# Kernel optimization log

Hardware: AMD Instinct MI355X
Metric: run time of the kernel (lower is better)

Reference implementation:

```python
import jax, jax.numpy as jnp
import numpy as np


def _lstm(x, Wk, Wr, b, reverse, return_seq):
    # Keras LSTM with activation='relu', recurrent_activation='sigmoid'.
    # Wk: (F, 4H), Wr: (H, 4H), b: (4H). Gate order: i, f, c, o.
    if reverse:
        x = jnp.flip(x, 1)
    H = Wr.shape[0]
    xg = jnp.einsum('btf,fg->btg', x, Wk) + b  # (B, T, 4H)
    B = x.shape[0]

    def step(carry, g_t):
        h, c = carry
        g = g_t + h @ Wr
        i = jax.nn.sigmoid(g[:, :H])
        f = jax.nn.sigmoid(g[:, H:2 * H])
        cc = jax.nn.relu(g[:, 2 * H:3 * H])
        o = jax.nn.sigmoid(g[:, 3 * H:])
        c = f * c + i * cc
        h = o * jax.nn.relu(c)
        return (h, c), h

    init = (jnp.zeros((B, H), x.dtype), jnp.zeros((B, H), x.dtype))
    (h, _), hs = jax.lax.scan(step, init, jnp.swapaxes(xg, 0, 1))
    if return_seq:
        hs = jnp.swapaxes(hs, 0, 1)  # (B, T, H)
        if reverse:
            hs = jnp.flip(hs, 1)
        return hs
    return h


def setup_inputs() -> dict:
    key = jax.random.key(0)
    ks = jax.random.split(key, 24)
    B, LA, T, F = 256, 200, 512, 128
    s = 0.05
    d = {
        'inputA': jax.random.randint(ks[0], (B, LA), 0, 1000),
        'inputB': jax.random.normal(ks[1], (B, T, F), jnp.float32),
        'emb': jax.random.normal(ks[2], (1000, 3), jnp.float32) * s,
        'w1': jax.random.normal(ks[3], (600, 256), jnp.float32) * s,
        'b1': jnp.zeros((256,), jnp.float32),
        'w2': jax.random.normal(ks[4], (256, 128), jnp.float32) * s,
        'b2': jnp.zeros((128,), jnp.float32),
        'w3': jax.random.normal(ks[5], (128, 64), jnp.float32) * s,
        'b3': jnp.zeros((64,), jnp.float32),
        'k1f': jax.random.normal(ks[6], (128, 512), jnp.float32) * s,
        'r1f': jax.random.normal(ks[7], (128, 512), jnp.float32) * s,
        'bb1f': jnp.zeros((512,), jnp.float32),
        'k1b': jax.random.normal(ks[8], (128, 512), jnp.float32) * s,
        'r1b': jax.random.normal(ks[9], (128, 512), jnp.float32) * s,
        'bb1b': jnp.zeros((512,), jnp.float32),
        'k2f': jax.random.normal(ks[10], (256, 256), jnp.float32) * s,
        'r2f': jax.random.normal(ks[11], (64, 256), jnp.float32) * s,
        'bb2f': jnp.zeros((256,), jnp.float32),
        'k2b': jax.random.normal(ks[12], (256, 256), jnp.float32) * s,
        'r2b': jax.random.normal(ks[13], (64, 256), jnp.float32) * s,
        'bb2b': jnp.zeros((256,), jnp.float32),
        'wz1': jax.random.normal(ks[14], (192, 2), jnp.float32) * s,
        'bz1': jnp.zeros((2,), jnp.float32),
        'wz2': jax.random.normal(ks[15], (2, 1), jnp.float32) * s,
        'bz2': jnp.zeros((1,), jnp.float32),
        'wt1': jax.random.normal(ks[16], (192, 2), jnp.float32) * s,
        'bt1': jnp.zeros((2,), jnp.float32),
        'wt2': jax.random.normal(ks[17], (2, 1), jnp.float32) * s,
        'bt2': jnp.zeros((1,), jnp.float32),
    }
    return d


def reference(inputA, inputB, emb, w1, b1, w2, b2, w3, b3,
              k1f, r1f, bb1f, k1b, r1b, bb1b,
              k2f, r2f, bb2f, k2b, r2b, bb2b,
              wz1, bz1, wz2, bz2, wt1, bt1, wt2, bt2):
    B = inputA.shape[0]
    # Embedding branch
    x = emb[inputA]                       # (B, LA, 3)
    x = x.reshape(B, -1)                  # flatten -> (B, 600)
    x = jax.nn.relu(x @ w1 + b1)
    x = jax.nn.relu(x @ w2 + b2)
    x = jax.nn.relu(x @ w3 + b3)          # (B, 64)
    # BiLSTM branch
    y_f = _lstm(inputB, k1f, r1f, bb1f, reverse=False, return_seq=True)
    y_b = _lstm(inputB, k1b, r1b, bb1b, reverse=True, return_seq=True)
    y = jnp.concatenate([y_f, y_b], axis=-1)   # (B, T, 256)
    h_f = _lstm(y, k2f, r2f, bb2f, reverse=False, return_seq=False)
    h_b = _lstm(y, k2b, r2b, bb2b, reverse=True, return_seq=False)
    y = jnp.concatenate([h_f, h_b], axis=-1)    # (B, 128)
    combined = jnp.concatenate([x, y], axis=-1)  # (B, 192)
    z = jax.nn.relu(combined @ wz1 + bz1) @ wz2 + bz2
    t = jax.nn.relu(combined @ wt1 + bt1) @ wt2 + bt2
    return (z, t)
```

## Files before the change

kernel.cpp:

```cpp
#include <hip/hip_runtime.h>

typedef __attribute__((ext_vector_type(8))) short s8v;
typedef __attribute__((ext_vector_type(4))) short s4v;
typedef __attribute__((ext_vector_type(4))) float f4v;
typedef __attribute__((ext_vector_type(4))) unsigned u4v;

#if __has_builtin(__builtin_amdgcn_exp2f)
#define EXP2(x) __builtin_amdgcn_exp2f(x)
#else
#define EXP2(x) exp2f(x)
#endif
#if __has_builtin(__builtin_amdgcn_rcpf)
#define RCP(x) __builtin_amdgcn_rcpf(x)
#else
#define RCP(x) (1.0f/(x))
#endif

#define LOG2E 1.4426950408889634f

__device__ __forceinline__ short f2bf(float f) {
    union { float f; unsigned u; } x; x.f = f;
    unsigned r = (x.u + 0x7FFFu + ((x.u >> 16) & 1u)) >> 16;
    return (short)r;
}
__device__ __forceinline__ float bflo(unsigned u) {
    union { unsigned u; float f; } x; x.u = u << 16; return x.f;
}
__device__ __forceinline__ float bfhi(unsigned u) {
    union { unsigned u; float f; } x; x.u = u & 0xffff0000u; return x.f;
}
__device__ __forceinline__ unsigned cvt_pk_bf16(float lo, float hi) {
    unsigned r;
    asm("v_cvt_pk_bf16_f32 %0, %1, %2" : "=v"(r) : "v"(lo), "v"(hi));
    return r;
}
__device__ __forceinline__ void lds_barrier() {
    asm volatile("s_waitcnt lgkmcnt(0)\n\ts_barrier" ::: "memory");
}

__global__ __launch_bounds__(256) void prep_embed_kernel(
        const float* __restrict__ k1f, const float* __restrict__ r1f,
        const float* __restrict__ k1b, const float* __restrict__ r1b,
        const float* __restrict__ k2f, const float* __restrict__ r2f,
        const float* __restrict__ k2b, const float* __restrict__ r2b,
        short* __restrict__ WB1, short* __restrict__ WB2,
        const int* __restrict__ inputA, const float* __restrict__ emb,
        const float* __restrict__ w1, const float* __restrict__ b1,
        const float* __restrict__ w2, const float* __restrict__ b2,
        const float* __restrict__ w3, const float* __restrict__ b3,
        float* __restrict__ xe) {
    if (blockIdx.x < 1024) {
        int idx = blockIdx.x * 256 + threadIdx.x;
        if (idx < 262144) {
            int j = idx & 7, l = (idx >> 3) & 63, c = (idx >> 9) & 7, n = (idx >> 12) & 31, d = (idx >> 17) & 1;
            int coln = n * 16 + (l & 15);
            int k = c * 32 + ((l >> 4) * 8) + j;
            const float* Wk = d ? k1b : k1f;
            const float* Wr = d ? r1b : r1f;
            float v = (c < 4) ? Wk[k * 512 + coln] : Wr[(k - 128) * 512 + coln];
            float sc = ((n >> 3) == 2) ? 1.0f : -LOG2E;
            WB1[idx] = f2bf(v * sc);
        }
        if (idx < 163840) {
            int d = idx / 81920, r0 = idx % 81920;
            int n = r0 / 5120, r1 = r0 % 5120;
            int c = r1 / 512, li = r1 % 512;
            int l = li >> 3, j = li & 7;
            int coln = n * 16 + (l & 15);
            int k = c * 32 + ((l >> 4) * 8) + j;
            const float* Wk = d ? k2b : k2f;
            const float* Wr = d ? r2b : r2f;
            float v = (k < 256) ? Wk[k * 256 + coln] : Wr[(k - 256) * 256 + coln];
            float sc = ((n >> 2) == 2) ? 1.0f : -LOG2E;
            WB2[idx] = f2bf(v * sc);
        }
        return;
    }
    __shared__ __align__(16) float row2[600][8];
    __shared__ __align__(16) float h1r[256][8];
    __shared__ __align__(16) float h2r[128][8];
    int blk = blockIdx.x - 1024;
    int b0 = blk * 8;
    int t = threadIdx.x;
    for (int i = t; i < 1600; i += 256) {
        int r = i / 200, p = i - r * 200;
        int idx = inputA[(b0 + r) * 200 + p];
        row2[p * 3 + 0][r] = emb[idx * 3 + 0];
        row2[p * 3 + 1][r] = emb[idx * 3 + 1];
        row2[p * 3 + 2][r] = emb[idx * 3 + 2];
    }
    __syncthreads();
    {
        float acc[8];
        float bv = b1[t];
#pragma unroll
        for (int r = 0; r < 8; r++) acc[r] = bv;
        for (int k = 0; k < 600; k++) {
            float wv = w1[k * 256 + t];
            const f4v* rp = (const f4v*)&row2[k][0];
            f4v r0 = rp[0], r1 = rp[1];
#pragma unroll
            for (int r = 0; r < 4; r++) acc[r] = fmaf(r0[r], wv, acc[r]);
#pragma unroll
            for (int r = 0; r < 4; r++) acc[4 + r] = fmaf(r1[r], wv, acc[4 + r]);
        }
#pragma unroll
        for (int r = 0; r < 8; r++) h1r[t][r] = fmaxf(acc[r], 0.f);
    }
    __syncthreads();
    if (t < 128) {
        float acc[8];
        float bv = b2[t];
#pragma unroll
        for (int r = 0; r < 8; r++) acc[r] = bv;
        for (int k = 0; k < 256; k++) {
            float wv = w2[k * 128 + t];
            const f4v* rp = (const f4v*)&h1r[k][0];
            f4v r0 = rp[0], r1 = rp[1];
#pragma unroll
            for (int r = 0; r < 4; r++) acc[r] = fmaf(r0[r], wv, acc[r]);
#pragma unroll
            for (int r = 0; r < 4; r++) acc[4 + r] = fmaf(r1[r], wv, acc[4 + r]);
        }
#pragma unroll
        for (int r = 0; r < 8; r++) h2r[t][r] = fmaxf(acc[r], 0.f);
    }
    __syncthreads();
    if (t < 64) {
        float acc[8];
        float bv = b3[t];
#pragma unroll
        for (int r = 0; r < 8; r++) acc[r] = bv;
        for (int k = 0; k < 128; k++) {
            float wv = w3[k * 64 + t];
            const f4v* rp = (const f4v*)&h2r[k][0];
            f4v r0 = rp[0], r1 = rp[1];
#pragma unroll
            for (int r = 0; r < 4; r++) acc[r] = fmaf(r0[r], wv, acc[r]);
#pragma unroll
            for (int r = 0; r < 4; r++) acc[4 + r] = fmaf(r1[r], wv, acc[4 + r]);
        }
#pragma unroll
        for (int r = 0; r < 8; r++) xe[(b0 + r) * 64 + t] = fmaxf(acc[r], 0.f);
    }
}

__global__ __launch_bounds__(512, 2) void megastep(
        const float* __restrict__ x, const short* __restrict__ WB1, const short* __restrict__ WB2,
        const float* __restrict__ bb1f, const float* __restrict__ bb1b,
        const float* __restrict__ bb2f, const float* __restrict__ bb2b,
        short* __restrict__ yfr, short* __restrict__ xgA, short* __restrict__ xgB,
        short* __restrict__ ygA, short* __restrict__ ygB,
        float* __restrict__ c1st, short* __restrict__ h1st,
        float* __restrict__ c2st, short* __restrict__ h2st,
        float* __restrict__ h2o, int k, int TC, int NC) {
    __shared__ short hA[2048];
    __shared__ short hB[2048];
    __shared__ __align__(16) short stg[38912];
    const int tid = threadIdx.x, lane = tid & 63, w = tid >> 6;
    const int bid = blockIdx.x;
    const int tgn = TC >> 3;

    if (bid < 32) {
        const int cl = k - 1;
        if (cl < 0 || cl >= NC) return;
        const int t0 = cl * TC;
        const int first = (cl == 0);
        const int btile = bid & 15, dir = bid >> 4;
        const int col = lane & 15, q = lane >> 4, u = (w << 4) + col;
        const int sb = dir * 16 + btile;

        s8v wf[4][4];
#pragma unroll
        for (int ti = 0; ti < 4; ti++)
#pragma unroll
            for (int c = 0; c < 4; c++)
                wf[ti][c] = *(const s8v*)(WB1 + ((((dir * 32 + (w + 8 * ti)) * 8) + 4 + c) * 64 + lane) * 8);

        float cst[4];
        if (first) {
#pragma unroll
            for (int r = 0; r < 4; r++) cst[r] = 0.f;
            for (int i = tid; i < 2048; i += 512) hA[i] = 0;
        } else {
            f4v cv = *(const f4v*)(c1st + ((size_t)sb * 8 + w) * 256 + lane * 4);
#pragma unroll
            for (int r = 0; r < 4; r++) cst[r] = cv[r];
            for (int i = tid; i < 2048; i += 512) hA[i] = h1st[sb * 2048 + i];
        }
        __syncthreads();

        const short* xgp = ((cl & 1) ? xgB : xgA) + (size_t)sb * TC * 8192 + w * 1024 + lane * 8;
        u4v pe0 = *(const u4v*)(xgp);
        u4v pe1 = *(const u4v*)(xgp + 512);
        u4v po0 = *(const u4v*)(xgp + 8192);
        u4v po1 = *(const u4v*)(xgp + 8192 + 512);

        const int hidx = (w >> 1) * 512 + ((u >> 3) & 3) * 128 + (u & 7);

        for (int s = 0; s < TC; s += 2) {
            {
                s8v ah[4];
#pragma unroll
                for (int cc = 0; cc < 4; cc++) ah[cc] = *(const s8v*)&hA[(cc * 64 + lane) * 8];
                f4v acc[4];
                acc[0][0] = bflo(pe0[0]); acc[0][1] = bfhi(pe0[0]); acc[0][2] = bflo(pe0[1]); acc[0][3] = bfhi(pe0[1]);
                acc[1][0] = bflo(pe0[2]); acc[1][1] = bfhi(pe0[2]); acc[1][2] = bflo(pe0[3]); acc[1][3] = bfhi(pe0[3]);
                acc[2][0] = bflo(pe1[0]); acc[2][1] = bfhi(pe1[0]); acc[2][2] = bflo(pe1[1]); acc[2][3] = bfhi(pe1[1]);
                acc[3][0] = bflo(pe1[2]); acc[3][1] = bfhi(pe1[2]); acc[3][2] = bflo(pe1[3]); acc[3][3] = bfhi(pe1[3]);
                {
                    const short* np = xgp + (size_t)(s + 2) * 8192;
                    pe0 = *(const u4v*)np;
                    pe1 = *(const u4v*)(np + 512);
                }
#pragma unroll
                for (int cc = 0; cc < 4; cc++)
#pragma unroll
                    for (int ti = 0; ti < 4; ti++)
                        acc[ti] = __builtin_amdgcn_mfma_f32_16x16x32_bf16(ah[cc], wf[ti][cc], acc[ti], 0, 0, 0);
                if (w >= 4 && s > 0) {
                    int tp = t0 + s - 1;
                    if (dir) tp = 511 - tp;
                    s8v hv = (w == 4) ? ah[0] : (w == 5) ? ah[1] : (w == 6) ? ah[2] : ah[3];
                    *(s8v*)(yfr + (((size_t)(btile * 512 + tp) * 8) + dir * 4 + (w - 4)) * 512 + lane * 8) = hv;
                }
                float hv_[4];
#pragma unroll
                for (int r = 0; r < 4; r++) {
                    float Ei = EXP2(acc[0][r]);
                    float Ef = EXP2(acc[1][r]);
                    float Eo = EXP2(acc[3][r]);
                    float rv = fmaxf(acc[2][r], 0.f);
                    float di = 1.f + Ei, df = 1.f + Ef;
                    float cn = fmaf(cst[r], di, rv * df) * RCP(di * df);
                    cst[r] = cn;
                    hv_[r] = fmaxf(cn, 0.f) * RCP(1.f + Eo);
                }
                unsigned p01 = cvt_pk_bf16(hv_[0], hv_[1]);
                unsigned p23 = cvt_pk_bf16(hv_[2], hv_[3]);
                short* hb = &hB[hidx + (q << 5)];
                hb[0]  = (short)p01;  hb[8]  = (short)(p01 >> 16);
                hb[16] = (short)p23;  hb[24] = (short)(p23 >> 16);
                lds_barrier();
            }
            {
                s8v ah[4];
#pragma unroll
                for (int cc = 0; cc < 4; cc++) ah[cc] = *(const s8v*)&hB[(cc * 64 + lane) * 8];
                f4v acc[4];
                acc[0][0] = bflo(po0[0]); acc[0][1] = bfhi(po0[0]); acc[0][2] = bflo(po0[1]); acc[0][3] = bfhi(po0[1]);
                acc[1][0] = bflo(po0[2]); acc[1][1] = bfhi(po0[2]); acc[1][2] = bflo(po0[3]); acc[1][3] = bfhi(po0[3]);
                acc[2][0] = bflo(po1[0]); acc[2][1] = bfhi(po1[0]); acc[2][2] = bflo(po1[1]); acc[2][3] = bfhi(po1[1]);
                acc[3][0] = bflo(po1[2]); acc[3][1] = bfhi(po1[2]); acc[3][2] = bflo(po1[3]); acc[3][3] = bfhi(po1[3]);
                {
                    const short* np = xgp + (size_t)(s + 3) * 8192;
                    po0 = *(const u4v*)np;
                    po1 = *(const u4v*)(np + 512);
                }
#pragma unroll
                for (int cc = 0; cc < 4; cc++)
#pragma unroll
                    for (int ti = 0; ti < 4; ti++)
                        acc[ti] = __builtin_amdgcn_mfma_f32_16x16x32_bf16(ah[cc], wf[ti][cc], acc[ti], 0, 0, 0);
                if (w >= 4) {
                    int tp = t0 + s;
                    if (dir) tp = 511 - tp;
                    s8v hv = (w == 4) ? ah[0] : (w == 5) ? ah[1] : (w == 6) ? ah[2] : ah[3];
                    *(s8v*)(yfr + (((size_t)(btile * 512 + tp) * 8) + dir * 4 + (w - 4)) * 512 + lane * 8) = hv;
                }
                float hv_[4];
#pragma unroll
                for (int r = 0; r < 4; r++) {
                    float Ei = EXP2(acc[0][r]);
                    float Ef = EXP2(acc[1][r]);
                    float Eo = EXP2(acc[3][r]);
                    float rv = fmaxf(acc[2][r], 0.f);
                    float di = 1.f + Ei, df = 1.f + Ef;
                    float cn = fmaf(cst[r], di, rv * df) * RCP(di * df);
                    cst[r] = cn;
                    hv_[r] = fmaxf(cn, 0.f) * RCP(1.f + Eo);
                }
                unsigned p01 = cvt_pk_bf16(hv_[0], hv_[1]);
                unsigned p23 = cvt_pk_bf16(hv_[2], hv_[3]);
                short* hb = &hA[hidx + (q << 5)];
                hb[0]  = (short)p01;  hb[8]  = (short)(p01 >> 16);
                hb[16] = (short)p23;  hb[24] = (short)(p23 >> 16);
                lds_barrier();
            }
        }
        if (w >= 4) {
            int tp = t0 + TC - 1;
            if (dir) tp = 511 - tp;
            s8v hv = *(const s8v*)&hA[((w - 4) * 64 + lane) * 8];
            *(s8v*)(yfr + (((size_t)(btile * 512 + tp) * 8) + dir * 4 + (w - 4)) * 512 + lane * 8) = hv;
        }
        f4v cv;
#pragma unroll
        for (int r = 0; r < 4; r++) cv[r] = cst[r];
        *(f4v*)(c1st + ((size_t)sb * 8 + w) * 256 + lane * 4) = cv;
        for (int i = tid; i < 2048; i += 512) h1st[sb * 2048 + i] = hA[i];
        return;
    }

    if (bid < 64) {
        const int c2 = k - 3;
        if (c2 < 0 || c2 >= NC) return;
        const int first = (c2 == 0), last = (c2 == NC - 1);
        const int btile = (bid - 32) & 15, dir = (bid - 32) >> 4;
        const int b0 = btile << 4;
        const int w4 = w & 3;
        const int col = lane & 15, q = lane >> 4, u = (w4 << 4) + col;
        const int sb = dir * 16 + btile;

        s8v wf[4][2];
#pragma unroll
        for (int ti = 0; ti < 4; ti++)
#pragma unroll
            for (int c = 0; c < 2; c++)
                wf[ti][c] = *(const s8v*)(WB2 + ((((dir * 16 + (w4 + 4 * ti)) * 10) + 8 + c) * 64 + lane) * 8);

        float cst[4], hl[4] = {0.f, 0.f, 0.f, 0.f};
        if (first) {
#pragma unroll
            for (int r = 0; r < 4; r++) cst[r] = 0.f;
            for (int i = tid; i < 1024; i += 512) hA[i] = 0;
        } else {
            f4v cv = *(const f4v*)(c2st + ((size_t)sb * 4 + w4) * 256 + lane * 4);
#pragma unroll
            for (int r = 0; r < 4; r++) cst[r] = cv[r];
            for (int i = tid; i < 1024; i += 512) hA[i] = h2st[sb * 1024 + i];
        }
        __syncthreads();

        const short* ygp = ((c2 & 1) ? ygB : ygA) + (size_t)sb * TC * 4096 + w4 * 1024 + lane * 8;
        u4v pe0, pe1, po0, po1;
        if (w < 4) {
            pe0 = *(const u4v*)(ygp);
            pe1 = *(const u4v*)(ygp + 512);
            po0 = *(const u4v*)(ygp + 4096);
            po1 = *(const u4v*)(ygp + 4096 + 512);
        }
        const int hidx = (w4 >> 1) * 512 + ((u >> 3) & 3) * 128 + (u & 7);

        for (int s = 0; s < TC; s += 2) {
            if (w < 4) {
                s8v ah[2];
#pragma unroll
                for (int cc = 0; cc < 2; cc++) ah[cc] = *(const s8v*)&hA[(cc * 64 + lane) * 8];
                f4v acc[4];
                acc[0][0] = bflo(pe0[0]); acc[0][1] = bfhi(pe0[0]); acc[0][2] = bflo(pe0[1]); acc[0][3] = bfhi(pe0[1]);
                acc[1][0] = bflo(pe0[2]); acc[1][1] = bfhi(pe0[2]); acc[1][2] = bflo(pe0[3]); acc[1][3] = bfhi(pe0[3]);
                acc[2][0] = bflo(pe1[0]); acc[2][1] = bfhi(pe1[0]); acc[2][2] = bflo(pe1[1]); acc[2][3] = bfhi(pe1[1]);
                acc[3][0] = bflo(pe1[2]); acc[3][1] = bfhi(pe1[2]); acc[3][2] = bflo(pe1[3]); acc[3][3] = bfhi(pe1[3]);
                {
                    const short* np = ygp + (size_t)(s + 2) * 4096;
                    pe0 = *(const u4v*)np;
                    pe1 = *(const u4v*)(np + 512);
                }
#pragma unroll
                for (int cc = 0; cc < 2; cc++)
#pragma unroll
                    for (int ti = 0; ti < 4; ti++)
                        acc[ti] = __builtin_amdgcn_mfma_f32_16x16x32_bf16(ah[cc], wf[ti][cc], acc[ti], 0, 0, 0);
#pragma unroll
                for (int r = 0; r < 4; r++) {
                    float Ei = EXP2(acc[0][r]);
                    float Ef = EXP2(acc[1][r]);
                    float Eo = EXP2(acc[3][r]);
                    float rv = fmaxf(acc[2][r], 0.f);
                    float di = 1.f + Ei, df = 1.f + Ef;
                    float cn = fmaf(cst[r], di, rv * df) * RCP(di * df);
                    cst[r] = cn;
                    hl[r] = fmaxf(cn, 0.f) * RCP(1.f + Eo);
                }
                unsigned p01 = cvt_pk_bf16(hl[0], hl[1]);
                unsigned p23 = cvt_pk_bf16(hl[2], hl[3]);
                short* hb = &hB[hidx + (q << 5)];
                hb[0]  = (short)p01;  hb[8]  = (short)(p01 >> 16);
                hb[16] = (short)p23;  hb[24] = (short)(p23 >> 16);
            }
            lds_barrier();
            if (w < 4) {
                s8v ah[2];
#pragma unroll
                for (int cc = 0; cc < 2; cc++) ah[cc] = *(const s8v*)&hB[(cc * 64 + lane) * 8];
                f4v acc[4];
                acc[0][0] = bflo(po0[0]); acc[0][1] = bfhi(po0[0]); acc[0][2] = bflo(po0[1]); acc[0][3] = bfhi(po0[1]);
                acc[1][0] = bflo(po0[2]); acc[1][1] = bfhi(po0[2]); acc[1][2] = bflo(po0[3]); acc[1][3] = bfhi(po0[3]);
                acc[2][0] = bflo(po1[0]); acc[2][1] = bfhi(po1[0]); acc[2][2] = bflo(po1[1]); acc[2][3] = bfhi(po1[1]);
                acc[3][0] = bflo(po1[2]); acc[3][1] = bfhi(po1[2]); acc[3][2] = bflo(po1[3]); acc[3][3] = bfhi(po1[3]);
                {
                    const short* np = ygp + (size_t)(s + 3) * 4096;
                    po0 = *(const u4v*)np;
                    po1 = *(const u4v*)(np + 512);
                }
#pragma unroll
                for (int cc = 0; cc < 2; cc++)
#pragma unroll
                    for (int ti = 0; ti < 4; ti++)
                        acc[ti] = __builtin_amdgcn_mfma_f32_16x16x32_bf16(ah[cc], wf[ti][cc], acc[ti], 0, 0, 0);
#pragma unroll
                for (int r = 0; r < 4; r++) {
                    float Ei = EXP2(acc[0][r]);
                    float Ef = EXP2(acc[1][r]);
                    float Eo = EXP2(acc[3][r]);
                    float rv = fmaxf(acc[2][r], 0.f);
                    float di = 1.f + Ei, df = 1.f + Ef;
                    float cn = fmaf(cst[r], di, rv * df) * RCP(di * df);
                    cst[r] = cn;
                    hl[r] = fmaxf(cn, 0.f) * RCP(1.f + Eo);
                }
                unsigned p01 = cvt_pk_bf16(hl[0], hl[1]);
                unsigned p23 = cvt_pk_bf16(hl[2], hl[3]);
                short* hb = &hA[hidx + (q << 5)];
                hb[0]  = (short)p01;  hb[8]  = (short)(p01 >> 16);
                hb[16] = (short)p23;  hb[24] = (short)(p23 >> 16);
            }
            lds_barrier();
        }
        if (w < 4) {
            f4v cv;
#pragma unroll
            for (int r = 0; r < 4; r++) cv[r] = cst[r];
            *(f4v*)(c2st + ((size_t)sb * 4 + w4) * 256 + lane * 4) = cv;
        }
        __syncthreads();
        for (int i = tid; i < 1024; i += 512) h2st[sb * 1024 + i] = hA[i];
        if (last && w < 4) {
#pragma unroll
            for (int r = 0; r < 4; r++)
                h2o[((dir * 256) + b0 + q * 4 + r) * 64 + u] = hl[r];
        }
        return;
    }

    if (bid < 64 + 4 * TC) {
        const int cg = k;
        if (cg >= NC) return;
        const int t0 = cg * TC;
        const int g = bid - 64;
        const int btile = g & 15;
        const int rest = g >> 4;
        const int tg = rest % tgn;
        const int dir = rest / tgn;
        const int b0 = btile << 4;
        short* xg_w = (cg & 1) ? xgB : xgA;
        {
            int tglob = t0 + tg * 8 + w;
            if (dir) tglob = 511 - tglob;
            const int half = lane >> 5;
            const int f0 = (lane & 31) * 4;
            const int cx = f0 >> 5, qq = (f0 >> 3) & 3, j0 = f0 & 7;
#pragma unroll
            for (int rr = 0; rr < 8; rr++) {
                const int m = rr * 2 + half;
                const float* xp = x + ((size_t)(b0 + m) * 512 + tglob) * 128 + f0;
                f4v v4 = *(const f4v*)xp;
                const int slot = (qq << 4) | ((m ^ qq ^ (cx << 1)) & 15);
                s4v pk;
#pragma unroll
                for (int j = 0; j < 4; j++) pk[j] = f2bf(v4[j]);
                *(s4v*)&stg[(((w * 4 + cx) * 64 + slot) * 8) + j0] = pk;
            }
        }
        s8v wf[4][4];
#pragma unroll
        for (int ti = 0; ti < 4; ti++)
#pragma unroll
            for (int c = 0; c < 4; c++)
                wf[ti][c] = *(const s8v*)(WB1 + ((((dir * 32 + (w + 8 * ti)) * 8) + c) * 64 + lane) * 8);
        const float* bb = dir ? bb1b : bb1f;
        float bias[4];
#pragma unroll
        for (int ti = 0; ti < 4; ti++) {
            const int tile = w + 8 * ti;
            float sc = ((tile >> 3) == 2) ? 1.0f : -LOG2E;
            bias[ti] = sc * bb[tile * 16 + (lane & 15)];
        }
        __syncthreads();
        const size_t sb = dir * 16 + btile;
#pragma unroll 2
        for (int sl = 0; sl < 8; sl++) {
            s8v a[4];
#pragma unroll
            for (int c = 0; c < 4; c++) {
                const int slot = lane ^ (lane >> 4) ^ (c << 1);
                a[c] = *(const s8v*)&stg[((sl * 4 + c) * 64 + slot) * 8];
            }
            f4v acc[4];
#pragma unroll
            for (int ti = 0; ti < 4; ti++) { f4v z = {0.f, 0.f, 0.f, 0.f}; acc[ti] = z; }
#pragma unroll
            for (int c = 0; c < 4; c++)
#pragma unroll
                for (int ti = 0; ti < 4; ti++)
                    acc[ti] = __builtin_amdgcn_mfma_f32_16x16x32_bf16(a[c], wf[ti][c], acc[ti], 0, 0, 0);
            short* outp = xg_w + ((sb * TC + (size_t)(tg * 8 + sl)) * 8 + w) * 1024 + lane * 8;
#pragma unroll
            for (int p = 0; p < 2; p++) {
                s8v v;
#pragma unroll
                for (int j = 0; j < 4; j++) {
                    v[j]     = f2bf(acc[2 * p][j]     + bias[2 * p]);
                    v[4 + j] = f2bf(acc[2 * p + 1][j] + bias[2 * p + 1]);
                }
                *(s8v*)(outp + p * 512) = v;
            }
        }
        return;
    }

    {
        const int cg = k - 2;
        if (cg < 0 || cg >= NC) return;
        const int t0 = cg * TC;
        const int g = bid - 64 - 4 * TC;
        const int btile = g & 15;
        const int rest = g >> 4;
        const int tg = rest % tgn;
        const int dir = rest / tgn;
        short* yg_w = (cg & 1) ? ygB : ygA;
        const int w4 = w & 3, sh = (w >> 2) * 4;
        s8v wf[4][8];
#pragma unroll
        for (int ti = 0; ti < 4; ti++)
#pragma unroll
            for (int c = 0; c < 8; c++)
                wf[ti][c] = *(const s8v*)(WB2 + ((((dir * 16 + (w4 + 4 * ti)) * 10) + c) * 64 + lane) * 8);
        const float* bb = dir ? bb2b : bb2f;
        float bias[4];
#pragma unroll
        for (int ti = 0; ti < 4; ti++) {
            const int tile = w4 + 4 * ti;
            float sc = ((tile >> 2) == 2) ? 1.0f : -LOG2E;
            bias[ti] = sc * bb[tile * 16 + (lane & 15)];
        }
        const size_t sb = dir * 16 + btile;
#pragma unroll
        for (int si = 0; si < 4; si++) {
            const int sl = sh + si;
            int tglob = t0 + tg * 8 + sl;
            if (dir) tglob = 511 - tglob;
            s8v a[8];
#pragma unroll
            for (int c = 0; c < 8; c++)
                a[c] = *(const s8v*)(yfr + (((size_t)(btile * 512 + tglob) * 8) + c) * 512 + lane * 8);
            f4v acc[4];
#pragma unroll
            for (int ti = 0; ti < 4; ti++) { f4v z = {0.f, 0.f, 0.f, 0.f}; acc[ti] = z; }
#pragma unroll
            for (int c = 0; c < 8; c++)
#pragma unroll
                for (int ti = 0; ti < 4; ti++)
                    acc[ti] = __builtin_amdgcn_mfma_f32_16x16x32_bf16(a[c], wf[ti][c], acc[ti], 0, 0, 0);
            short* outp = yg_w + ((sb * TC + (size_t)(tg * 8 + sl)) * 4 + w4) * 1024 + lane * 8;
#pragma unroll
            for (int p = 0; p < 2; p++) {
                s8v v;
#pragma unroll
                for (int j = 0; j < 4; j++) {
                    v[j]     = f2bf(acc[2 * p][j]     + bias[2 * p]);
                    v[4 + j] = f2bf(acc[2 * p + 1][j] + bias[2 * p + 1]);
                }
                *(s8v*)(outp + p * 512) = v;
            }
        }
    }
}

__global__ void heads_kernel(const float* __restrict__ xe, const float* __restrict__ h2o,
                             const float* __restrict__ wz1, const float* __restrict__ bz1,
                             const float* __restrict__ wz2, const float* __restrict__ bz2,
                             const float* __restrict__ wt1, const float* __restrict__ bt1,
                             const float* __restrict__ wt2, const float* __restrict__ bt2,
                             float* __restrict__ out) {
    int b = threadIdx.x;
    float cz0 = bz1[0], cz1 = bz1[1], ct0 = bt1[0], ct1 = bt1[1];
    for (int k = 0; k < 192; k++) {
        float v = (k < 64) ? xe[b * 64 + k]
                : (k < 128) ? h2o[b * 64 + (k - 64)]
                            : h2o[(256 + b) * 64 + (k - 128)];
        cz0 += v * wz1[k * 2 + 0];
        cz1 += v * wz1[k * 2 + 1];
        ct0 += v * wt1[k * 2 + 0];
        ct1 += v * wt1[k * 2 + 1];
    }
    cz0 = fmaxf(cz0, 0.f); cz1 = fmaxf(cz1, 0.f);
    ct0 = fmaxf(ct0, 0.f); ct1 = fmaxf(ct1, 0.f);
    out[b] = cz0 * wz2[0] + cz1 * wz2[1] + bz2[0];
    out[256 + b] = ct0 * wt2[0] + ct1 * wt2[1] + bt2[0];
}

extern "C" void kernel_launch(void* const* d_in, const int* in_sizes, int n_in,
                              void* d_out, int out_size, void* d_ws, size_t ws_size,
                              hipStream_t stream) {
    const int*   inputA = (const int*)d_in[0];
    const float* inputB = (const float*)d_in[1];
    const float* emb = (const float*)d_in[2];
    const float* w1  = (const float*)d_in[3];
    const float* b1  = (const float*)d_in[4];
    const float* w2  = (const float*)d_in[5];
    const float* b2  = (const float*)d_in[6];
    const float* w3  = (const float*)d_in[7];
    const float* b3  = (const float*)d_in[8];
    const float* k1f = (const float*)d_in[9];
    const float* r1f = (const float*)d_in[10];
    const float* bb1f= (const float*)d_in[11];
    const float* k1b = (const float*)d_in[12];
    const float* r1b = (const float*)d_in[13];
    const float* bb1b= (const float*)d_in[14];
    const float* k2f = (const float*)d_in[15];
    const float* r2f = (const float*)d_in[16];
    const float* bb2f= (const float*)d_in[17];
    const float* k2b = (const float*)d_in[18];
    const float* r2b = (const float*)d_in[19];
    const float* bb2b= (const float*)d_in[20];
    const float* wz1 = (const float*)d_in[21];
    const float* bz1 = (const float*)d_in[22];
    const float* wz2 = (const float*)d_in[23];
    const float* bz2 = (const float*)d_in[24];
    const float* wt1 = (const float*)d_in[25];
    const float* bt1 = (const float*)d_in[26];
    const float* wt2 = (const float*)d_in[27];
    const float* bt2 = (const float*)d_in[28];

    char* ws = (char*)d_ws;
    short* WB1  = (short*)(ws);
    short* WB2  = (short*)(ws + 524288);
    float* xe   = (float*)(ws + 851968);
    float* h2o  = (float*)(ws + 917504);
    float* c1st = (float*)(ws + 1048576);
    short* h1st = (short*)(ws + 1310720);
    float* c2st = (float*)(ws + 1441792);
    short* h2st = (short*)(ws + 1572864);
    short* yfr  = (short*)(ws + 2097152);
    float* out  = (float*)d_out;

    const int TC = 32;
    const int NC = 512 / TC;
    short* xgA = (short*)(ws + 69206016);
    short* xgB = xgA + (size_t)TC * 262144;
    short* ygA = xgB + (size_t)TC * 262144;
    short* ygB = ygA + (size_t)TC * 131072;
    const int grid = 64 + 8 * TC;

    prep_embed_kernel<<<1056, 256, 0, stream>>>(k1f, r1f, k1b, r1b, k2f, r2f, k2b, r2b,
                                                WB1, WB2, inputA, emb, w1, b1, w2, b2, w3, b3, xe);
    for (int k = 0; k < NC + 3; k++) {
        megastep<<<grid, 512, 0, stream>>>(inputB, WB1, WB2, bb1f, bb1b, bb2f, bb2b,
                                           yfr, xgA, xgB, ygA, ygB,
                                           c1st, h1st, c2st, h2st, h2o, k, TC, NC);
    }
    heads_kernel<<<1, 256, 0, stream>>>(xe, h2o, wz1, bz1, wz2, bz2, wt1, bt1, wt2, bt2, out);
}
```

Baseline: 681.8 us.

## Move embedding MLP into idle blocks of the final megastep launch

Strips the embedding-branch MLP out of the prep kernel, so prep only repacks the LSTM weights. The MLP now runs inside the last megastep launch on blocks 64-95, which would otherwise return immediately while the second LSTM layer finishes its recurrence. Each layer's K dimension is split across all 512 threads, and partial sums are reduced through shared memory. This takes the serial MLP off the critical path at startup, at the cost of a longer megastep parameter list and more shared-memory reductions and barriers.

```diff
diff --git a/kernel.cpp b/kernel.cpp
--- a/kernel.cpp
+++ b/kernel.cpp
@@ -38,110 +38,35 @@
     asm volatile("s_waitcnt lgkmcnt(0)\n\ts_barrier" ::: "memory");
 }
 
-__global__ __launch_bounds__(256) void prep_embed_kernel(
+__global__ __launch_bounds__(512) void prep_kernel(
         const float* __restrict__ k1f, const float* __restrict__ r1f,
         const float* __restrict__ k1b, const float* __restrict__ r1b,
         const float* __restrict__ k2f, const float* __restrict__ r2f,
         const float* __restrict__ k2b, const float* __restrict__ r2b,
-        short* __restrict__ WB1, short* __restrict__ WB2,
-        const int* __restrict__ inputA, const float* __restrict__ emb,
-        const float* __restrict__ w1, const float* __restrict__ b1,
-        const float* __restrict__ w2, const float* __restrict__ b2,
-        const float* __restrict__ w3, const float* __restrict__ b3,
-        float* __restrict__ xe) {
-    if (blockIdx.x < 1024) {
-        int idx = blockIdx.x * 256 + threadIdx.x;
-        if (idx < 262144) {
-            int j = idx & 7, l = (idx >> 3) & 63, c = (idx >> 9) & 7, n = (idx >> 12) & 31, d = (idx >> 17) & 1;
-            int coln = n * 16 + (l & 15);
-            int k = c * 32 + ((l >> 4) * 8) + j;
-            const float* Wk = d ? k1b : k1f;
-            const float* Wr = d ? r1b : r1f;
-            float v = (c < 4) ? Wk[k * 512 + coln] : Wr[(k - 128) * 512 + coln];
-            float sc = ((n >> 3) == 2) ? 1.0f : -LOG2E;
-            WB1[idx] = f2bf(v * sc);
-        }
-        if (idx < 163840) {
-            int d = idx / 81920, r0 = idx % 81920;
-            int n = r0 / 5120, r1 = r0 % 5120;
-            int c = r1 / 512, li = r1 % 512;
-            int l = li >> 3, j = li & 7;
-            int coln = n * 16 + (l & 15);
-            int k = c * 32 + ((l >> 4) * 8) + j;
-            const float* Wk = d ? k2b : k2f;
-            const float* Wr = d ? r2b : r2f;
-            float v = (k < 256) ? Wk[k * 256 + coln] : Wr[(k - 256) * 256 + coln];
-            float sc = ((n >> 2) == 2) ? 1.0f : -LOG2E;
-            WB2[idx] = f2bf(v * sc);
-        }
-        return;
-    }
-    __shared__ __align__(16) float row2[600][8];
-    __shared__ __align__(16) float h1r[256][8];
-    __shared__ __align__(16) float h2r[128][8];
-    int blk = blockIdx.x - 1024;
-    int b0 = blk * 8;
-    int t = threadIdx.x;
-    for (int i = t; i < 1600; i += 256) {
-        int r = i / 200, p = i - r * 200;
-        int idx = inputA[(b0 + r) * 200 + p];
-        row2[p * 3 + 0][r] = emb[idx * 3 + 0];
-        row2[p * 3 + 1][r] = emb[idx * 3 + 1];
-        row2[p * 3 + 2][r] = emb[idx * 3 + 2];
-    }
-    __syncthreads();
-    {
-        float acc[8];
-        float bv = b1[t];
-#pragma unroll
-        for (int r = 0; r < 8; r++) acc[r] = bv;
-        for (int k = 0; k < 600; k++) {
-            float wv = w1[k * 256 + t];
-            const f4v* rp = (const f4v*)&row2[k][0];
-            f4v r0 = rp[0], r1 = rp[1];
-#pragma unroll
-            for (int r = 0; r < 4; r++) acc[r] = fmaf(r0[r], wv, acc[r]);
-#pragma unroll
-            for (int r = 0; r < 4; r++) acc[4 + r] = fmaf(r1[r], wv, acc[4 + r]);
-        }
-#pragma unroll
-        for (int r = 0; r < 8; r++) h1r[t][r] = fmaxf(acc[r], 0.f);
-    }
-    __syncthreads();
-    if (t < 128) {
-        float acc[8];
-        float bv = b2[t];
-#pragma unroll
-        for (int r = 0; r < 8; r++) acc[r] = bv;
-        for (int k = 0; k < 256; k++) {
-            float wv = w2[k * 128 + t];
-            const f4v* rp = (const f4v*)&h1r[k][0];
-            f4v r0 = rp[0], r1 = rp[1];
-#pragma unroll
-            for (int r = 0; r < 4; r++) acc[r] = fmaf(r0[r], wv, acc[r]);
-#pragma unroll
-            for (int r = 0; r < 4; r++) acc[4 + r] = fmaf(r1[r], wv, acc[4 + r]);
-        }
-#pragma unroll
-        for (int r = 0; r < 8; r++) h2r[t][r] = fmaxf(acc[r], 0.f);
-    }
-    __syncthreads();
-    if (t < 64) {
-        float acc[8];
-        float bv = b3[t];
-#pragma unroll
-        for (int r = 0; r < 8; r++) acc[r] = bv;
-        for (int k = 0; k < 128; k++) {
-            float wv = w3[k * 64 + t];
-            const f4v* rp = (const f4v*)&h2r[k][0];
-            f4v r0 = rp[0], r1 = rp[1];
-#pragma unroll
-            for (int r = 0; r < 4; r++) acc[r] = fmaf(r0[r], wv, acc[r]);
-#pragma unroll
-            for (int r = 0; r < 4; r++) acc[4 + r] = fmaf(r1[r], wv, acc[4 + r]);
-        }
-#pragma unroll
-        for (int r = 0; r < 8; r++) xe[(b0 + r) * 64 + t] = fmaxf(acc[r], 0.f);
+        short* __restrict__ WB1, short* __restrict__ WB2) {
+    int idx = blockIdx.x * 512 + threadIdx.x;
+    if (idx < 262144) {
+        int j = idx & 7, l = (idx >> 3) & 63, c = (idx >> 9) & 7, n = (idx >> 12) & 31, d = (idx >> 17) & 1;
+        int coln = n * 16 + (l & 15);
+        int k = c * 32 + ((l >> 4) * 8) + j;
+        const float* Wk = d ? k1b : k1f;
+        const float* Wr = d ? r1b : r1f;
+        float v = (c < 4) ? Wk[k * 512 + coln] : Wr[(k - 128) * 512 + coln];
+        float sc = ((n >> 3) == 2) ? 1.0f : -LOG2E;
+        WB1[idx] = f2bf(v * sc);
+    }
+    if (idx < 163840) {
+        int d = idx / 81920, r0 = idx % 81920;
+        int n = r0 / 5120, r1 = r0 % 5120;
+        int c = r1 / 512, li = r1 % 512;
+        int l = li >> 3, j = li & 7;
+        int coln = n * 16 + (l & 15);
+        int k = c * 32 + ((l >> 4) * 8) + j;
+        const float* Wk = d ? k2b : k2f;
+        const float* Wr = d ? r2b : r2f;
+        float v = (k < 256) ? Wk[k * 256 + coln] : Wr[(k - 256) * 256 + coln];
+        float sc = ((n >> 2) == 2) ? 1.0f : -LOG2E;
+        WB2[idx] = f2bf(v * sc);
     }
 }
 
@@ -153,7 +78,13 @@
         short* __restrict__ ygA, short* __restrict__ ygB,
         float* __restrict__ c1st, short* __restrict__ h1st,
         float* __restrict__ c2st, short* __restrict__ h2st,
-        float* __restrict__ h2o, int k, int TC, int NC) {
+        float* __restrict__ h2o,
+        const int* __restrict__ inputA, const float* __restrict__ emb,
+        const float* __restrict__ w1, const float* __restrict__ b1,
+        const float* __restrict__ w2, const float* __restrict__ b2,
+        const float* __restrict__ w3, const float* __restrict__ b3,
+        float* __restrict__ xe,
+        int k, int TC, int NC) {
     __shared__ short hA[2048];
     __shared__ short hB[2048];
     __shared__ __align__(16) short stg[38912];
@@ -430,6 +361,117 @@
 #pragma unroll
             for (int r = 0; r < 4; r++)
                 h2o[((dir * 256) + b0 + q * 4 + r) * 64 + u] = hl[r];
+        }
+        return;
+    }
+
+    if (k == NC + 2) {
+        if (bid >= 96) return;
+        float* fl   = (float*)stg;
+        float* row2 = fl;
+        float* h1r  = fl + 4800;
+        float* h2r  = fl + 6848;
+        float* part = fl + 7872;
+        const int blk = bid - 64;
+        const int b0 = blk * 8;
+        for (int i = tid; i < 1600; i += 512) {
+            int r = i / 200, p = i - r * 200;
+            int idx = inputA[(b0 + r) * 200 + p];
+            row2[(p * 3 + 0) * 8 + r] = emb[idx * 3 + 0];
+            row2[(p * 3 + 1) * 8 + r] = emb[idx * 3 + 1];
+            row2[(p * 3 + 2) * 8 + r] = emb[idx * 3 + 2];
+        }
+        __syncthreads();
+        {
+            const int kc = tid >> 8, t = tid & 255;
+            float acc[8];
+#pragma unroll
+            for (int r = 0; r < 8; r++) acc[r] = 0.f;
+            const int k0 = kc * 300;
+#pragma unroll 4
+            for (int kk = 0; kk < 300; kk++) {
+                float wv = w1[(k0 + kk) * 256 + t];
+                const f4v* rp = (const f4v*)&row2[(k0 + kk) * 8];
+                f4v r0 = rp[0], r1 = rp[1];
+#pragma unroll
+                for (int r = 0; r < 4; r++) acc[r] = fmaf(r0[r], wv, acc[r]);
+#pragma unroll
+                for (int r = 0; r < 4; r++) acc[4 + r] = fmaf(r1[r], wv, acc[4 + r]);
+            }
+            if (kc == 1) {
+#pragma unroll
+                for (int r = 0; r < 8; r++) part[t * 8 + r] = acc[r];
+            }
+            __syncthreads();
+            if (kc == 0) {
+                float bv = b1[t];
+#pragma unroll
+                for (int r = 0; r < 8; r++) h1r[t * 8 + r] = fmaxf(acc[r] + part[t * 8 + r] + bv, 0.f);
+            }
+        }
+        __syncthreads();
+        {
+            const int kc = tid >> 7, t = tid & 127;
+            float acc[8];
+#pragma unroll
+            for (int r = 0; r < 8; r++) acc[r] = 0.f;
+            const int k0 = kc * 64;
+#pragma unroll 4
+            for (int kk = 0; kk < 64; kk++) {
+                float wv = w2[(k0 + kk) * 128 + t];
+                const f4v* rp = (const f4v*)&h1r[(k0 + kk) * 8];
+                f4v r0 = rp[0], r1 = rp[1];
+#pragma unroll
+                for (int r = 0; r < 4; r++) acc[r] = fmaf(r0[r], wv, acc[r]);
+#pragma unroll
+                for (int r = 0; r < 4; r++) acc[4 + r] = fmaf(r1[r], wv, acc[4 + r]);
+            }
+            if (kc > 0) {
+#pragma unroll
+                for (int r = 0; r < 8; r++) part[((kc - 1) * 128 + t) * 8 + r] = acc[r];
+            }
+            __syncthreads();
+            if (kc == 0) {
+                float bv = b2[t];
+#pragma unroll
+                for (int r = 0; r < 8; r++) {
+                    float v = acc[r] + part[(t) * 8 + r] + part[(128 + t) * 8 + r] + part[(256 + t) * 8 + r] + bv;
+                    h2r[t * 8 + r] = fmaxf(v, 0.f);
+                }
+            }
+        }
+        __syncthreads();
+        {
+            const int kc = tid >> 6, t = tid & 63;
+            float acc[8];
+#pragma unroll
+            for (int r = 0; r < 8; r++) acc[r] = 0.f;
+            const int k0 = kc * 16;
+#pragma unroll
+            for (int kk = 0; kk < 16; kk++) {
+                float wv = w3[(k0 + kk) * 64 + t];
+                const f4v* rp = (const f4v*)&h2r[(k0 + kk) * 8];
+                f4v r0 = rp[0], r1 = rp[1];
+#pragma unroll
+                for (int r = 0; r < 4; r++) acc[r] = fmaf(r0[r], wv, acc[r]);
+#pragma unroll
+                for (int r = 0; r < 4; r++) acc[4 + r] = fmaf(r1[r], wv, acc[4 + r]);
+            }
+            if (kc > 0) {
+#pragma unroll
+                for (int r = 0; r < 8; r++) part[((kc - 1) * 64 + t) * 8 + r] = acc[r];
+            }
+            __syncthreads();
+            if (kc == 0) {
+                float bv = b3[t];
+#pragma unroll
+                for (int r = 0; r < 8; r++) {
+                    float v = acc[r] + bv;
+#pragma unroll
+                    for (int j = 0; j < 7; j++) v += part[(j * 64 + t) * 8 + r];
+                    xe[(b0 + r) * 64 + t] = fmaxf(v, 0.f);
+                }
+            }
         }
         return;
     }
@@ -644,12 +686,13 @@
     short* ygB = ygA + (size_t)TC * 131072;
     const int grid = 64 + 8 * TC;
 
-    prep_embed_kernel<<<1056, 256, 0, stream>>>(k1f, r1f, k1b, r1b, k2f, r2f, k2b, r2b,
-                                                WB1, WB2, inputA, emb, w1, b1, w2, b2, w3, b3, xe);
+    prep_kernel<<<512, 512, 0, stream>>>(k1f, r1f, k1b, r1b, k2f, r2f, k2b, r2b, WB1, WB2);
     for (int k = 0; k < NC + 3; k++) {
         megastep<<<grid, 512, 0, stream>>>(inputB, WB1, WB2, bb1f, bb1b, bb2f, bb2b,
                                            yfr, xgA, xgB, ygA, ygB,
-                                           c1st, h1st, c2st, h2st, h2o, k, TC, NC);
+                                           c1st, h1st, c2st, h2st, h2o,
+                                           inputA, emb, w1, b1, w2, b2, w3, b3, xe,
+                                           k, TC, NC);
     }
     heads_kernel<<<1, 256, 0, stream>>>(xe, h2o, wz1, bz1, wz2, bz2, wt1, bt1, wt2, bt2, out);
 }
```

Result: no change. 688.8 us (+1.0%).

## Move embedding MLP branch into idle megastep blocks during pipeline drain

Applied to the files above, without the earlier changes.

The embedding-branch MLP (gather plus three dense layers) is taken out of the prep kernel and run inside the megastep launch where k equals NC. At that step the x-gate projection blocks have no chunk to process, and they are otherwise idle. Each of 128 blocks computes two batch rows using the shared staging buffer, so this work overlaps the recurrent stages instead of sitting on the critical path before them. The prep kernel now only repacks weights, using 512-thread blocks. The MLP uses fewer rows per block, so weight loads are reused less, and it may lengthen that megastep if those blocks end up finishing last.

```diff
diff --git a/kernel.cpp b/kernel.cpp
--- a/kernel.cpp
+++ b/kernel.cpp
@@ -38,110 +38,35 @@
     asm volatile("s_waitcnt lgkmcnt(0)\n\ts_barrier" ::: "memory");
 }
 
-__global__ __launch_bounds__(256) void prep_embed_kernel(
+__global__ __launch_bounds__(512) void prep_kernel(
         const float* __restrict__ k1f, const float* __restrict__ r1f,
         const float* __restrict__ k1b, const float* __restrict__ r1b,
         const float* __restrict__ k2f, const float* __restrict__ r2f,
         const float* __restrict__ k2b, const float* __restrict__ r2b,
-        short* __restrict__ WB1, short* __restrict__ WB2,
-        const int* __restrict__ inputA, const float* __restrict__ emb,
-        const float* __restrict__ w1, const float* __restrict__ b1,
-        const float* __restrict__ w2, const float* __restrict__ b2,
-        const float* __restrict__ w3, const float* __restrict__ b3,
-        float* __restrict__ xe) {
-    if (blockIdx.x < 1024) {
-        int idx = blockIdx.x * 256 + threadIdx.x;
-        if (idx < 262144) {
-            int j = idx & 7, l = (idx >> 3) & 63, c = (idx >> 9) & 7, n = (idx >> 12) & 31, d = (idx >> 17) & 1;
-            int coln = n * 16 + (l & 15);
-            int k = c * 32 + ((l >> 4) * 8) + j;
-            const float* Wk = d ? k1b : k1f;
-            const float* Wr = d ? r1b : r1f;
-            float v = (c < 4) ? Wk[k * 512 + coln] : Wr[(k - 128) * 512 + coln];
-            float sc = ((n >> 3) == 2) ? 1.0f : -LOG2E;
-            WB1[idx] = f2bf(v * sc);
-        }
-        if (idx < 163840) {
-            int d = idx / 81920, r0 = idx % 81920;
-            int n = r0 / 5120, r1 = r0 % 5120;
-            int c = r1 / 512, li = r1 % 512;
-            int l = li >> 3, j = li & 7;
-            int coln = n * 16 + (l & 15);
-            int k = c * 32 + ((l >> 4) * 8) + j;
-            const float* Wk = d ? k2b : k2f;
-            const float* Wr = d ? r2b : r2f;
-            float v = (k < 256) ? Wk[k * 256 + coln] : Wr[(k - 256) * 256 + coln];
-            float sc = ((n >> 2) == 2) ? 1.0f : -LOG2E;
-            WB2[idx] = f2bf(v * sc);
-        }
-        return;
-    }
-    __shared__ __align__(16) float row2[600][8];
-    __shared__ __align__(16) float h1r[256][8];
-    __shared__ __align__(16) float h2r[128][8];
-    int blk = blockIdx.x - 1024;
-    int b0 = blk * 8;
-    int t = threadIdx.x;
-    for (int i = t; i < 1600; i += 256) {
-        int r = i / 200, p = i - r * 200;
-        int idx = inputA[(b0 + r) * 200 + p];
-        row2[p * 3 + 0][r] = emb[idx * 3 + 0];
-        row2[p * 3 + 1][r] = emb[idx * 3 + 1];
-        row2[p * 3 + 2][r] = emb[idx * 3 + 2];
-    }
-    __syncthreads();
-    {
-        float acc[8];
-        float bv = b1[t];
-#pragma unroll
-        for (int r = 0; r < 8; r++) acc[r] = bv;
-        for (int k = 0; k < 600; k++) {
-            float wv = w1[k * 256 + t];
-            const f4v* rp = (const f4v*)&row2[k][0];
-            f4v r0 = rp[0], r1 = rp[1];
-#pragma unroll
-            for (int r = 0; r < 4; r++) acc[r] = fmaf(r0[r], wv, acc[r]);
-#pragma unroll
-            for (int r = 0; r < 4; r++) acc[4 + r] = fmaf(r1[r], wv, acc[4 + r]);
-        }
-#pragma unroll
-        for (int r = 0; r < 8; r++) h1r[t][r] = fmaxf(acc[r], 0.f);
-    }
-    __syncthreads();
-    if (t < 128) {
-        float acc[8];
-        float bv = b2[t];
-#pragma unroll
-        for (int r = 0; r < 8; r++) acc[r] = bv;
-        for (int k = 0; k < 256; k++) {
-            float wv = w2[k * 128 + t];
-            const f4v* rp = (const f4v*)&h1r[k][0];
-            f4v r0 = rp[0], r1 = rp[1];
-#pragma unroll
-            for (int r = 0; r < 4; r++) acc[r] = fmaf(r0[r], wv, acc[r]);
-#pragma unroll
-            for (int r = 0; r < 4; r++) acc[4 + r] = fmaf(r1[r], wv, acc[4 + r]);
-        }
-#pragma unroll
-        for (int r = 0; r < 8; r++) h2r[t][r] = fmaxf(acc[r], 0.f);
-    }
-    __syncthreads();
-    if (t < 64) {
-        float acc[8];
-        float bv = b3[t];
-#pragma unroll
-        for (int r = 0; r < 8; r++) acc[r] = bv;
-        for (int k = 0; k < 128; k++) {
-            float wv = w3[k * 64 + t];
-            const f4v* rp = (const f4v*)&h2r[k][0];
-            f4v r0 = rp[0], r1 = rp[1];
-#pragma unroll
-            for (int r = 0; r < 4; r++) acc[r] = fmaf(r0[r], wv, acc[r]);
-#pragma unroll
-            for (int r = 0; r < 4; r++) acc[4 + r] = fmaf(r1[r], wv, acc[4 + r]);
-        }
-#pragma unroll
-        for (int r = 0; r < 8; r++) xe[(b0 + r) * 64 + t] = fmaxf(acc[r], 0.f);
+        short* __restrict__ WB1, short* __restrict__ WB2) {
+    int idx = blockIdx.x * 512 + threadIdx.x;
+    if (idx < 262144) {
+        int j = idx & 7, l = (idx >> 3) & 63, c = (idx >> 9) & 7, n = (idx >> 12) & 31, d = (idx >> 17) & 1;
+        int coln = n * 16 + (l & 15);
+        int k = c * 32 + ((l >> 4) * 8) + j;
+        const float* Wk = d ? k1b : k1f;
+        const float* Wr = d ? r1b : r1f;
+        float v = (c < 4) ? Wk[k * 512 + coln] : Wr[(k - 128) * 512 + coln];
+        float sc = ((n >> 3) == 2) ? 1.0f : -LOG2E;
+        WB1[idx] = f2bf(v * sc);
+    }
+    if (idx < 163840) {
+        int d = idx / 81920, r0 = idx % 81920;
+        int n = r0 / 5120, r1 = r0 % 5120;
+        int c = r1 / 512, li = r1 % 512;
+        int l = li >> 3, j = li & 7;
+        int coln = n * 16 + (l & 15);
+        int k = c * 32 + ((l >> 4) * 8) + j;
+        const float* Wk = d ? k2b : k2f;
+        const float* Wr = d ? r2b : r2f;
+        float v = (k < 256) ? Wk[k * 256 + coln] : Wr[(k - 256) * 256 + coln];
+        float sc = ((n >> 2) == 2) ? 1.0f : -LOG2E;
+        WB2[idx] = f2bf(v * sc);
     }
 }
 
@@ -153,7 +78,13 @@
         short* __restrict__ ygA, short* __restrict__ ygB,
         float* __restrict__ c1st, short* __restrict__ h1st,
         float* __restrict__ c2st, short* __restrict__ h2st,
-        float* __restrict__ h2o, int k, int TC, int NC) {
+        float* __restrict__ h2o,
+        const int* __restrict__ inputA, const float* __restrict__ emb,
+        const float* __restrict__ w1, const float* __restrict__ b1,
+        const float* __restrict__ w2, const float* __restrict__ b2,
+        const float* __restrict__ w3, const float* __restrict__ b3,
+        float* __restrict__ xe,
+        int k, int TC, int NC) {
     __shared__ short hA[2048];
     __shared__ short hB[2048];
     __shared__ __align__(16) short stg[38912];
@@ -436,7 +367,47 @@
 
     if (bid < 64 + 4 * TC) {
         const int cg = k;
-        if (cg >= NC) return;
+        if (cg >= NC) {
+            if (k != NC) return;
+            float* fl   = (float*)stg;
+            float* rowv = fl;
+            float* h1v  = fl + 1200;
+            float* h2v  = fl + 1712;
+            const int rr = tid >> 8;
+            const int t  = tid & 255;
+            const int row = (bid - 64) * 2 + rr;
+            if (t < 200) {
+                int idx = inputA[row * 200 + t];
+                rowv[rr * 600 + t * 3 + 0] = emb[idx * 3 + 0];
+                rowv[rr * 600 + t * 3 + 1] = emb[idx * 3 + 1];
+                rowv[rr * 600 + t * 3 + 2] = emb[idx * 3 + 2];
+            }
+            __syncthreads();
+            {
+                float a = b1[t];
+                const float* rp = rowv + rr * 600;
+#pragma unroll 4
+                for (int kk = 0; kk < 600; kk++) a = fmaf(rp[kk], w1[kk * 256 + t], a);
+                h1v[rr * 256 + t] = fmaxf(a, 0.f);
+            }
+            __syncthreads();
+            if (t < 128) {
+                float a = b2[t];
+                const float* rp = h1v + rr * 256;
+#pragma unroll 4
+                for (int kk = 0; kk < 256; kk++) a = fmaf(rp[kk], w2[kk * 128 + t], a);
+                h2v[rr * 128 + t] = fmaxf(a, 0.f);
+            }
+            __syncthreads();
+            if (t < 64) {
+                float a = b3[t];
+                const float* rp = h2v + rr * 128;
+#pragma unroll 4
+                for (int kk = 0; kk < 128; kk++) a = fmaf(rp[kk], w3[kk * 64 + t], a);
+                xe[row * 64 + t] = fmaxf(a, 0.f);
+            }
+            return;
+        }
         const int t0 = cg * TC;
         const int g = bid - 64;
         const int btile = g & 15;
@@ -576,6 +547,7 @@
                              float* __restrict__ out) {
     int b = threadIdx.x;
     float cz0 = bz1[0], cz1 = bz1[1], ct0 = bt1[0], ct1 = bt1[1];
+#pragma unroll 4
     for (int k = 0; k < 192; k++) {
         float v = (k < 64) ? xe[b * 64 + k]
                 : (k < 128) ? h2o[b * 64 + (k - 64)]
@@ -644,12 +616,13 @@
     short* ygB = ygA + (size_t)TC * 131072;
     const int grid = 64 + 8 * TC;
 
-    prep_embed_kernel<<<1056, 256, 0, stream>>>(k1f, r1f, k1b, r1b, k2f, r2f, k2b, r2b,
-                                                WB1, WB2, inputA, emb, w1, b1, w2, b2, w3, b3, xe);
+    prep_kernel<<<512, 512, 0, stream>>>(k1f, r1f, k1b, r1b, k2f, r2f, k2b, r2b, WB1, WB2);
     for (int k = 0; k < NC + 3; k++) {
         megastep<<<grid, 512, 0, stream>>>(inputB, WB1, WB2, bb1f, bb1b, bb2f, bb2b,
                                            yfr, xgA, xgB, ygA, ygB,
-                                           c1st, h1st, c2st, h2st, h2o, k, TC, NC);
+                                           c1st, h1st, c2st, h2st, h2o,
+                                           inputA, emb, w1, b1, w2, b2, w3, b3, xe,
+                                           k, TC, NC);
     }
     heads_kernel<<<1, 256, 0, stream>>>(xe, h2o, wz1, bz1, wz2, bz2, wt1, bt1, wt2, bt2, out);
 }
```

After: 732.8 us. 7.5% more time.
